# Kernel optimization log

Hardware: AMD Instinct MI355X
Metric: run time of the kernel (lower is better)

## Reference

```python
import jax, jax.numpy as jnp
import numpy as np

H, W = 256, 832            # full-res organized point cloud (HEIGHT/WIDTH globals)
STRIDE_H, STRIDE_W = 2, 4  # stride_H_list[0], stride_W_list[0]
OUT_H, OUT_W = 128, 208    # out_H_list[0], out_W_list[0]
KH, KW = 12, 20            # layer0 kernel_size
K = 32                     # layer0 K_sample


def _sa_layer(pts, h_idx, w_idx, w1, b1, w2, b2, w3, b3):
    """PointNet SA: strided center selection, window KNN grouping, MLP, max-pool.
    pts: (B,H,W,3); h_idx/w_idx: (M,) full-res grid coords of selected centers.
    """
    B = pts.shape[0]
    pts_flat = pts.reshape(B, H * W, 3)
    center_idx = h_idx * W + w_idx                      # (M,)
    centers = pts_flat[:, center_idx]                   # (B,M,3)  fast_select gather
    # candidate window around each center (clipped at borders)
    dh = jnp.arange(KH) - KH // 2
    dw = jnp.arange(KW) - KW // 2
    cand_h = jnp.clip(h_idx[:, None] + dh, 0, H - 1)    # (M,KH)
    cand_w = jnp.clip(w_idx[:, None] + dw, 0, W - 1)    # (M,KW)
    cand_idx = (cand_h[:, :, None] * W + cand_w[:, None, :]).reshape(-1, KH * KW)  # (M,P)
    cand = pts_flat[:, cand_idx]                        # (B,M,P,3) irregular gather
    d2 = jnp.sum((cand - centers[:, :, None, :]) ** 2, axis=-1)  # (B,M,P)
    _, nn = jax.lax.top_k(-d2, K)                       # K nearest within window
    knn = jnp.take_along_axis(cand, nn[..., None], axis=2)       # (B,M,K,3)
    rel = knn - centers[:, :, None, :]                  # local coordinates
    h = jax.nn.relu(rel @ w1 + b1)                      # mlp [8,8,16]
    h = jax.nn.relu(h @ w2 + b2)
    h = jax.nn.relu(h @ w3 + b3)
    return centers, jnp.max(h, axis=2)                  # (B,M,3), (B,M,16)


def setup_inputs() -> dict:
    key = jax.random.key(0)
    ks = jax.random.split(key, 5)
    return {
        "pos1": jax.random.normal(ks[0], (2, H, W, 3), jnp.float32) * 5.0,
        "pos2": jax.random.normal(ks[1], (2, H, W, 3), jnp.float32) * 5.0,
        "w1": jax.random.normal(ks[2], (3, 8), jnp.float32) * 0.3,
        "b1": jnp.zeros((8,), jnp.float32),
        "w2": jax.random.normal(ks[3], (8, 8), jnp.float32) * 0.3,
        "b2": jnp.zeros((8,), jnp.float32),
        "w3": jax.random.normal(ks[4], (8, 16), jnp.float32) * 0.3,
        "b3": jnp.zeros((16,), jnp.float32),
    }


def reference(pos1, pos2, w1, b1, w2, b2, w3, b3):
    # get_selected_idx for level 0: strided grid subsampling
    h_idx = jnp.repeat(jnp.arange(OUT_H) * STRIDE_H, OUT_W)  # (M,)
    w_idx = jnp.tile(jnp.arange(OUT_W) * STRIDE_W, OUT_H)    # (M,)
    _, f1 = _sa_layer(pos1, h_idx, w_idx, w1, b1, w2, b2, w3, b3)
    _, f2 = _sa_layer(pos2, h_idx, w_idx, w1, b1, w2, b2, w3, b3)
    return jnp.concatenate([f1, f2], axis=-1)  # (B, OUT_H*OUT_W, 32)
```

## Files before the change

kernel.cpp:

```cpp
#include <hip/hip_runtime.h>
#include <hip/hip_bf16.h>

#define HH 256
#define WW 832
#define OHH 128
#define OWW 208
#define NCAND 240
#define MM (OHH*OWW)

typedef float v2f __attribute__((ext_vector_type(2)));

__device__ __forceinline__ int iclamp(int v, int lo, int hi) { return min(max(v, lo), hi); }
__device__ __forceinline__ int mbcnt64(unsigned long long m) {
    return __builtin_amdgcn_mbcnt_hi((unsigned)(m >> 32),
           __builtin_amdgcn_mbcnt_lo((unsigned)(m & 0xFFFFFFFFull), 0));
}
__device__ __forceinline__ v2f sxor(v2f v, int m) {
    v2f r; r.x = __shfl_xor(v.x, m); r.y = __shfl_xor(v.y, m); return r;
}

__global__ void __launch_bounds__(256) sa_fused(
    const float* __restrict__ pos1, const float* __restrict__ pos2,
    const float* __restrict__ w1, const float* __restrict__ b1,
    const float* __restrict__ w2, const float* __restrict__ b2,
    const float* __restrict__ w3, const float* __restrict__ b3,
    float* __restrict__ out)
{
    __shared__ v2f sW1p[3][4];
    __shared__ v2f sW2p[8][4];
    __shared__ v2f sW3p[8][8];
    __shared__ v2f sB1p[4], sB2p[4], sB3p[8];
    __shared__ float4 selRel[128];
    __shared__ int tIdx[256];
    __shared__ int tHW[256];

    const int t = threadIdx.x;
    { int kh = (t * 205) >> 12; int kw = t - kh * 20;
      tHW[t]  = (kh << 16) | kw;
      tIdx[t] = (t < NCAND) ? (kh * WW + kw) * 3 : 0; }
    if (t < 12)              { int i = t >> 2,  op = t & 3;
        sW1p[i][op] = (v2f){w1[i*8 + 2*op], w1[i*8 + 2*op + 1]}; }
    if (t >= 16 && t < 48)   { int u = t - 16, i = u >> 2, op = u & 3;
        sW2p[i][op] = (v2f){w2[i*8 + 2*op], w2[i*8 + 2*op + 1]}; }
    if (t >= 64 && t < 128)  { int u = t - 64, i = u >> 3, op = u & 7;
        sW3p[i][op] = (v2f){w3[i*16 + 2*op], w3[i*16 + 2*op + 1]}; }
    if (t >= 128 && t < 132) { int u = t - 128; sB1p[u] = (v2f){b1[2*u], b1[2*u + 1]}; }
    if (t >= 132 && t < 136) { int u = t - 132; sB2p[u] = (v2f){b2[2*u], b2[2*u + 1]}; }
    if (t >= 136 && t < 144) { int u = t - 136; sB3p[u] = (v2f){b3[2*u], b3[2*u + 1]}; }
    __syncthreads();

    const int lane = t & 63;
    const int wid  = t >> 6;
    const int m    = blockIdx.x * 4 + wid;
    const int b    = blockIdx.y & 1;
    const int cl   = blockIdx.y >> 1;
    const float* __restrict__ base = (cl ? pos2 : pos1) + (size_t)b * (HH * WW * 3);

    const unsigned um = (unsigned)m;
    const int oh = (int)(um / OWW);
    const int ow = (int)(um - (unsigned)oh * OWW);
    const int h0 = oh * 2, w0 = ow * 4;

    const float cx = base[(h0 * WW + w0) * 3 + 0];
    const float cy = base[(h0 * WW + w0) * 3 + 1];
    const float cz = base[(h0 * WW + w0) * 3 + 2];

    unsigned d2b[4];
    float dxv[4], dyv[4], dzv[4];
    const bool interior = ((unsigned)(oh - 3) <= 122u) && ((unsigned)(ow - 3) <= 202u);
    if (interior) {
        const float* wbase = base + ((h0 - 6) * WW + (w0 - 10)) * 3;
        #pragma unroll
        for (int q = 0; q < 4; ++q) {
            const float* p = wbase + tIdx[q * 64 + lane];
            float dx = __fsub_rn(p[0], cx);
            float dy = __fsub_rn(p[1], cy);
            float dz = __fsub_rn(p[2], cz);
            dxv[q] = dx; dyv[q] = dy; dzv[q] = dz;
            d2b[q] = __float_as_uint(__fadd_rn(__fadd_rn(__fmul_rn(dx, dx), __fmul_rn(dy, dy)), __fmul_rn(dz, dz)));
        }
    } else {
        #pragma unroll
        for (int q = 0; q < 4; ++q) {
            int hw = tHW[q * 64 + lane];
            int ch = iclamp(h0 - 6 + (hw >> 16), 0, HH - 1);
            int cw = iclamp(w0 - 10 + (hw & 0xFFFF), 0, WW - 1);
            const float* p = base + (ch * WW + cw) * 3;
            float dx = __fsub_rn(p[0], cx);
            float dy = __fsub_rn(p[1], cy);
            float dz = __fsub_rn(p[2], cz);
            dxv[q] = dx; dyv[q] = dy; dzv[q] = dz;
            d2b[q] = __float_as_uint(__fadd_rn(__fadd_rn(__fmul_rn(dx, dx), __fmul_rn(dy, dy)), __fmul_rn(dz, dz)));
        }
    }
    if (lane >= 48) d2b[3] = 0xFFFFFFFFu;

    unsigned T = 0;
    unsigned long long sm0 = 0, sm1 = 0, sm2 = 0, sm3 = 0;
    bool exact = false;
    for (int bpos = 30; bpos >= 0; --bpos) {
        unsigned Q = T | (1u << bpos);
        unsigned long long t0 = __ballot(d2b[0] < Q);
        unsigned long long t1 = __ballot(d2b[1] < Q);
        unsigned long long t2 = __ballot(d2b[2] < Q);
        unsigned long long t3 = __ballot(d2b[3] < Q);
        int c = __popcll(t0) + __popcll(t1) + __popcll(t2) + __popcll(t3);
        if (c == 32) { sm0 = t0; sm1 = t1; sm2 = t2; sm3 = t3; exact = true; break; }
        if (c < 32) T = Q;
    }
    if (!exact) {
        unsigned long long l0 = __ballot(d2b[0] < T);
        unsigned long long l1 = __ballot(d2b[1] < T);
        unsigned long long l2 = __ballot(d2b[2] < T);
        unsigned long long l3 = __ballot(d2b[3] < T);
        unsigned long long e0 = __ballot(d2b[0] == T);
        unsigned long long e1 = __ballot(d2b[1] == T);
        unsigned long long e2 = __ballot(d2b[2] == T);
        unsigned long long e3 = __ballot(d2b[3] == T);
        int c_lt = __popcll(l0) + __popcll(l1) + __popcll(l2) + __popcll(l3);
        int r = 32 - c_lt;
        int p1 = __popcll(e0), p2 = p1 + __popcll(e1), p3 = p2 + __popcll(e2);
        bool s0 = (d2b[0] < T) || ((d2b[0] == T) && (mbcnt64(e0) < r));
        bool s1 = (d2b[1] < T) || ((d2b[1] == T) && (p1 + mbcnt64(e1) < r));
        bool s2 = (d2b[2] < T) || ((d2b[2] == T) && (p2 + mbcnt64(e2) < r));
        bool s3 = (d2b[3] < T) || ((d2b[3] == T) && (p3 + mbcnt64(e3) < r));
        sm0 = __ballot(s0); sm1 = __ballot(s1); sm2 = __ballot(s2); sm3 = __ballot(s3);
    }

    {
        int c1 = __popcll(sm0);
        int c2 = c1 + __popcll(sm1);
        int c3 = c2 + __popcll(sm2);
        int lb = wid * 32;
        if ((sm0 >> lane) & 1) selRel[lb +      mbcnt64(sm0)] = make_float4(dxv[0], dyv[0], dzv[0], 0.f);
        if ((sm1 >> lane) & 1) selRel[lb + c1 + mbcnt64(sm1)] = make_float4(dxv[1], dyv[1], dzv[1], 0.f);
        if ((sm2 >> lane) & 1) selRel[lb + c2 + mbcnt64(sm2)] = make_float4(dxv[2], dyv[2], dzv[2], 0.f);
        if ((sm3 >> lane) & 1) selRel[lb + c3 + mbcnt64(sm3)] = make_float4(dxv[3], dyv[3], dzv[3], 0.f);
    }
    asm volatile("s_waitcnt lgkmcnt(0)" ::: "memory");
    __builtin_amdgcn_sched_barrier(0);

    {
        float4 rel = selRel[wid * 32 + (lane & 31)];
        v2f rx2 = (v2f){rel.x, rel.x};
        v2f ry2 = (v2f){rel.y, rel.y};
        v2f rz2 = (v2f){rel.z, rel.z};

        v2f a1[4];
        #pragma unroll
        for (int op = 0; op < 4; ++op) {
            v2f a = sB1p[op];
            a = __builtin_elementwise_fma(rx2, sW1p[0][op], a);
            a = __builtin_elementwise_fma(ry2, sW1p[1][op], a);
            a = __builtin_elementwise_fma(rz2, sW1p[2][op], a);
            a1[op] = __builtin_elementwise_max(a, (v2f)(0.f));
        }
        v2f a2[4];
        #pragma unroll
        for (int op = 0; op < 4; ++op) a2[op] = sB2p[op];
        #pragma unroll
        for (int i = 0; i < 8; ++i) {
            float h = a1[i >> 1][i & 1];
            v2f hb = (v2f){h, h};
            #pragma unroll
            for (int op = 0; op < 4; ++op)
                a2[op] = __builtin_elementwise_fma(hb, sW2p[i][op], a2[op]);
        }
        #pragma unroll
        for (int op = 0; op < 4; ++op) a2[op] = __builtin_elementwise_max(a2[op], (v2f)(0.f));

        const int obp = (lane >> 5) << 2;
        v2f a3[4];
        #pragma unroll
        for (int op = 0; op < 4; ++op) a3[op] = sB3p[obp + op];
        #pragma unroll
        for (int i = 0; i < 8; ++i) {
            float h = a2[i >> 1][i & 1];
            v2f hb = (v2f){h, h};
            #pragma unroll
            for (int op = 0; op < 4; ++op)
                a3[op] = __builtin_elementwise_fma(hb, sW3p[i][obp + op], a3[op]);
        }

        #pragma unroll
        for (int step = 16; step >= 1; step >>= 1) {
            #pragma unroll
            for (int op = 0; op < 4; ++op)
                a3[op] = __builtin_elementwise_max(a3[op], sxor(a3[op], step));
        }
        if ((lane & 31) == 0) {
            #pragma unroll
            for (int op = 0; op < 4; ++op)
                a3[op] = __builtin_elementwise_max(a3[op], (v2f)(0.f));
            const int ob = (lane >> 5) << 3;
            float4* dst = (float4*)(out + ((size_t)(b * MM + m) * 32) + (size_t)cl * 16 + ob);
            dst[0] = make_float4(a3[0].x, a3[0].y, a3[1].x, a3[1].y);
            dst[1] = make_float4(a3[2].x, a3[2].y, a3[3].x, a3[3].y);
        }
    }
}

extern "C" void kernel_launch(void* const* d_in, const int* in_sizes, int n_in,
                              void* d_out, int out_size, void* d_ws, size_t ws_size,
                              hipStream_t stream) {
    const float* pos1 = (const float*)d_in[0];
    const float* pos2 = (const float*)d_in[1];
    const float* w1   = (const float*)d_in[2];
    const float* b1   = (const float*)d_in[3];
    const float* w2   = (const float*)d_in[4];
    const float* b2   = (const float*)d_in[5];
    const float* w3   = (const float*)d_in[6];
    const float* b3   = (const float*)d_in[7];
    float* out = (float*)d_out;

    dim3 grid(MM / 4, 4);
    sa_fused<<<grid, 256, 0, stream>>>(pos1, pos2, w1, b1, w2, b2, w3, b3, out);
}
```

Measured before the change: 100.8 us.

## Process two centers per wavefront with half-wave split radix select

Each 64-lane wavefront now handles two output centers, one per 32-lane half, with each lane holding 8 candidates instead of 4. The bitwise threshold search runs both halves together using split ballot popcounts, and each lane computes all 16 output channels for its center instead of splitting channels across halves. This halves the grid size and cuts the share of a wave spent on padded candidates and on the MLP duplicated across channel halves. In exchange it raises register pressure (8 candidates per lane, 16 accumulators) and the shared selection loop runs until the slower of the two centers finishes.

```diff
diff --git a/kernel.cpp b/kernel.cpp
--- a/kernel.cpp
+++ b/kernel.cpp
@@ -11,9 +11,8 @@
 typedef float v2f __attribute__((ext_vector_type(2)));
 
 __device__ __forceinline__ int iclamp(int v, int lo, int hi) { return min(max(v, lo), hi); }
-__device__ __forceinline__ int mbcnt64(unsigned long long m) {
-    return __builtin_amdgcn_mbcnt_hi((unsigned)(m >> 32),
-           __builtin_amdgcn_mbcnt_lo((unsigned)(m & 0xFFFFFFFFull), 0));
+__device__ __forceinline__ int mbcnt2(unsigned lo, unsigned hi) {
+    return __builtin_amdgcn_mbcnt_hi(hi, __builtin_amdgcn_mbcnt_lo(lo, 0));
 }
 __device__ __forceinline__ v2f sxor(v2f v, int m) {
     v2f r; r.x = __shfl_xor(v.x, m); r.y = __shfl_xor(v.y, m); return r;
@@ -30,14 +29,9 @@
     __shared__ v2f sW2p[8][4];
     __shared__ v2f sW3p[8][8];
     __shared__ v2f sB1p[4], sB2p[4], sB3p[8];
-    __shared__ float4 selRel[128];
-    __shared__ int tIdx[256];
-    __shared__ int tHW[256];
+    __shared__ float4 selRel[256];
 
     const int t = threadIdx.x;
-    { int kh = (t * 205) >> 12; int kw = t - kh * 20;
-      tHW[t]  = (kh << 16) | kw;
-      tIdx[t] = (t < NCAND) ? (kh * WW + kw) * 3 : 0; }
     if (t < 12)              { int i = t >> 2,  op = t & 3;
         sW1p[i][op] = (v2f){w1[i*8 + 2*op], w1[i*8 + 2*op + 1]}; }
     if (t >= 16 && t < 48)   { int u = t - 16, i = u >> 2, op = u & 3;
@@ -51,97 +45,118 @@
 
     const int lane = t & 63;
     const int wid  = t >> 6;
-    const int m    = blockIdx.x * 4 + wid;
+    const int l31  = lane & 31;
+    const int half = lane >> 5;
+    const int m    = blockIdx.x * 8 + wid * 2 + half;
     const int b    = blockIdx.y & 1;
     const int cl   = blockIdx.y >> 1;
     const float* __restrict__ base = (cl ? pos2 : pos1) + (size_t)b * (HH * WW * 3);
 
-    const unsigned um = (unsigned)m;
-    const int oh = (int)(um / OWW);
-    const int ow = (int)(um - (unsigned)oh * OWW);
+    const int oh = (int)(((unsigned)(m >> 4) * 5042u) >> 16);
+    const int ow = m - oh * OWW;
     const int h0 = oh * 2, w0 = ow * 4;
 
-    const float cx = base[(h0 * WW + w0) * 3 + 0];
-    const float cy = base[(h0 * WW + w0) * 3 + 1];
-    const float cz = base[(h0 * WW + w0) * 3 + 2];
-
-    unsigned d2b[4];
-    float dxv[4], dyv[4], dzv[4];
+    const int cidx = (h0 * WW + w0) * 3;
+    const float cx = base[cidx + 0];
+    const float cy = base[cidx + 1];
+    const float cz = base[cidx + 2];
+
+    unsigned d2b[8];
+    float rxv[8], ryv[8], rzv[8];
     const bool interior = ((unsigned)(oh - 3) <= 122u) && ((unsigned)(ow - 3) <= 202u);
-    if (interior) {
-        const float* wbase = base + ((h0 - 6) * WW + (w0 - 10)) * 3;
-        #pragma unroll
-        for (int q = 0; q < 4; ++q) {
-            const float* p = wbase + tIdx[q * 64 + lane];
+    const bool allInt = (__ballot(interior) == ~0ull);
+    if (allInt) {
+        const float* wb = base + ((h0 - 6) * WW + (w0 - 10)) * 3;
+        #pragma unroll
+        for (int r = 0; r < 8; ++r) {
+            int j = r * 32 + l31;
+            if (r == 7) j = min(j, NCAND - 1);
+            int kh = (j * 205) >> 12;
+            int kw = j - kh * 20;
+            const float* p = wb + (kh * WW + kw) * 3;
             float dx = __fsub_rn(p[0], cx);
             float dy = __fsub_rn(p[1], cy);
             float dz = __fsub_rn(p[2], cz);
-            dxv[q] = dx; dyv[q] = dy; dzv[q] = dz;
-            d2b[q] = __float_as_uint(__fadd_rn(__fadd_rn(__fmul_rn(dx, dx), __fmul_rn(dy, dy)), __fmul_rn(dz, dz)));
+            rxv[r] = dx; ryv[r] = dy; rzv[r] = dz;
+            d2b[r] = __float_as_uint(__fadd_rn(__fadd_rn(__fmul_rn(dx, dx), __fmul_rn(dy, dy)), __fmul_rn(dz, dz)));
         }
     } else {
         #pragma unroll
-        for (int q = 0; q < 4; ++q) {
-            int hw = tHW[q * 64 + lane];
-            int ch = iclamp(h0 - 6 + (hw >> 16), 0, HH - 1);
-            int cw = iclamp(w0 - 10 + (hw & 0xFFFF), 0, WW - 1);
+        for (int r = 0; r < 8; ++r) {
+            int j = r * 32 + l31;
+            if (r == 7) j = min(j, NCAND - 1);
+            int kh = (j * 205) >> 12;
+            int kw = j - kh * 20;
+            int ch = iclamp(h0 - 6 + kh, 0, HH - 1);
+            int cw = iclamp(w0 - 10 + kw, 0, WW - 1);
             const float* p = base + (ch * WW + cw) * 3;
             float dx = __fsub_rn(p[0], cx);
             float dy = __fsub_rn(p[1], cy);
             float dz = __fsub_rn(p[2], cz);
-            dxv[q] = dx; dyv[q] = dy; dzv[q] = dz;
-            d2b[q] = __float_as_uint(__fadd_rn(__fadd_rn(__fmul_rn(dx, dx), __fmul_rn(dy, dy)), __fmul_rn(dz, dz)));
-        }
-    }
-    if (lane >= 48) d2b[3] = 0xFFFFFFFFu;
-
-    unsigned T = 0;
-    unsigned long long sm0 = 0, sm1 = 0, sm2 = 0, sm3 = 0;
-    bool exact = false;
+            rxv[r] = dx; ryv[r] = dy; rzv[r] = dz;
+            d2b[r] = __float_as_uint(__fadd_rn(__fadd_rn(__fmul_rn(dx, dx), __fmul_rn(dy, dy)), __fmul_rn(dz, dz)));
+        }
+    }
+    if (l31 >= 16) d2b[7] = 0xFFFFFFFFu;
+
+    unsigned TA = 0, TB = 0;
+    bool doneA = false, doneB = false;
     for (int bpos = 30; bpos >= 0; --bpos) {
-        unsigned Q = T | (1u << bpos);
-        unsigned long long t0 = __ballot(d2b[0] < Q);
-        unsigned long long t1 = __ballot(d2b[1] < Q);
-        unsigned long long t2 = __ballot(d2b[2] < Q);
-        unsigned long long t3 = __ballot(d2b[3] < Q);
-        int c = __popcll(t0) + __popcll(t1) + __popcll(t2) + __popcll(t3);
-        if (c == 32) { sm0 = t0; sm1 = t1; sm2 = t2; sm3 = t3; exact = true; break; }
-        if (c < 32) T = Q;
-    }
-    if (!exact) {
-        unsigned long long l0 = __ballot(d2b[0] < T);
-        unsigned long long l1 = __ballot(d2b[1] < T);
-        unsigned long long l2 = __ballot(d2b[2] < T);
-        unsigned long long l3 = __ballot(d2b[3] < T);
-        unsigned long long e0 = __ballot(d2b[0] == T);
-        unsigned long long e1 = __ballot(d2b[1] == T);
-        unsigned long long e2 = __ballot(d2b[2] == T);
-        unsigned long long e3 = __ballot(d2b[3] == T);
-        int c_lt = __popcll(l0) + __popcll(l1) + __popcll(l2) + __popcll(l3);
-        int r = 32 - c_lt;
-        int p1 = __popcll(e0), p2 = p1 + __popcll(e1), p3 = p2 + __popcll(e2);
-        bool s0 = (d2b[0] < T) || ((d2b[0] == T) && (mbcnt64(e0) < r));
-        bool s1 = (d2b[1] < T) || ((d2b[1] == T) && (p1 + mbcnt64(e1) < r));
-        bool s2 = (d2b[2] < T) || ((d2b[2] == T) && (p2 + mbcnt64(e2) < r));
-        bool s3 = (d2b[3] < T) || ((d2b[3] == T) && (p3 + mbcnt64(e3) < r));
-        sm0 = __ballot(s0); sm1 = __ballot(s1); sm2 = __ballot(s2); sm3 = __ballot(s3);
-    }
+        unsigned QA = doneA ? TA : (TA | (1u << bpos));
+        unsigned QB = doneB ? TB : (TB | (1u << bpos));
+        unsigned Qv = half ? QB : QA;
+        unsigned long long m0 = __ballot(d2b[0] < Qv);
+        unsigned long long m1 = __ballot(d2b[1] < Qv);
+        unsigned long long m2 = __ballot(d2b[2] < Qv);
+        unsigned long long m3 = __ballot(d2b[3] < Qv);
+        unsigned long long m4 = __ballot(d2b[4] < Qv);
+        unsigned long long m5 = __ballot(d2b[5] < Qv);
+        unsigned long long m6 = __ballot(d2b[6] < Qv);
+        unsigned long long m7 = __ballot(d2b[7] < Qv);
+        int cA = __popc((unsigned)m0) + __popc((unsigned)m1) + __popc((unsigned)m2) + __popc((unsigned)m3)
+               + __popc((unsigned)m4) + __popc((unsigned)m5) + __popc((unsigned)m6) + __popc((unsigned)m7);
+        int cB = __popc((unsigned)(m0 >> 32)) + __popc((unsigned)(m1 >> 32)) + __popc((unsigned)(m2 >> 32)) + __popc((unsigned)(m3 >> 32))
+               + __popc((unsigned)(m4 >> 32)) + __popc((unsigned)(m5 >> 32)) + __popc((unsigned)(m6 >> 32)) + __popc((unsigned)(m7 >> 32));
+        if (!doneA) { if (cA == 32) { TA = QA; doneA = true; } else if (cA < 32) TA = QA; }
+        if (!doneB) { if (cB == 32) { TB = QB; doneB = true; } else if (cB < 32) TB = QB; }
+        if (doneA && doneB) break;
+    }
+
+    const unsigned Tv = half ? TB : TA;
+
+    int cltA = 0, cltB = 0;
+    #pragma unroll
+    for (int r = 0; r < 8; ++r) {
+        unsigned long long lm = __ballot(d2b[r] < Tv);
+        cltA += __popc((unsigned)lm);
+        cltB += __popc((unsigned)(lm >> 32));
+    }
+    const int rv = half ? (32 - cltB) : (32 - cltA);
+    const unsigned hmLo = half ? 0u : 0xFFFFFFFFu;
+    const unsigned hmHi = half ? 0xFFFFFFFFu : 0u;
 
     {
-        int c1 = __popcll(sm0);
-        int c2 = c1 + __popcll(sm1);
-        int c3 = c2 + __popcll(sm2);
-        int lb = wid * 32;
-        if ((sm0 >> lane) & 1) selRel[lb +      mbcnt64(sm0)] = make_float4(dxv[0], dyv[0], dzv[0], 0.f);
-        if ((sm1 >> lane) & 1) selRel[lb + c1 + mbcnt64(sm1)] = make_float4(dxv[1], dyv[1], dzv[1], 0.f);
-        if ((sm2 >> lane) & 1) selRel[lb + c2 + mbcnt64(sm2)] = make_float4(dxv[2], dyv[2], dzv[2], 0.f);
-        if ((sm3 >> lane) & 1) selRel[lb + c3 + mbcnt64(sm3)] = make_float4(dxv[3], dyv[3], dzv[3], 0.f);
+        int peA = 0, peB = 0, psA = 0, psB = 0;
+        #pragma unroll
+        for (int r = 0; r < 8; ++r) {
+            bool eqr = (d2b[r] == Tv);
+            unsigned long long em = __ballot(eqr);
+            int pe = half ? peB : peA;
+            bool tie = eqr && (pe + mbcnt2((unsigned)em & hmLo, (unsigned)(em >> 32) & hmHi) < rv);
+            bool mine = (d2b[r] < Tv) || tie;
+            unsigned long long sm = __ballot(mine);
+            int ps = half ? psB : psA;
+            int rank = ps + mbcnt2((unsigned)sm & hmLo, (unsigned)(sm >> 32) & hmHi);
+            if (mine) selRel[wid * 64 + half * 32 + rank] = make_float4(rxv[r], ryv[r], rzv[r], 0.f);
+            peA += __popc((unsigned)em);  peB += __popc((unsigned)(em >> 32));
+            psA += __popc((unsigned)sm);  psB += __popc((unsigned)(sm >> 32));
+        }
     }
     asm volatile("s_waitcnt lgkmcnt(0)" ::: "memory");
     __builtin_amdgcn_sched_barrier(0);
 
     {
-        float4 rel = selRel[wid * 32 + (lane & 31)];
+        float4 rel = selRel[wid * 64 + lane];
         v2f rx2 = (v2f){rel.x, rel.x};
         v2f ry2 = (v2f){rel.y, rel.y};
         v2f rz2 = (v2f){rel.z, rel.z};
@@ -169,33 +184,33 @@
         #pragma unroll
         for (int op = 0; op < 4; ++op) a2[op] = __builtin_elementwise_max(a2[op], (v2f)(0.f));
 
-        const int obp = (lane >> 5) << 2;
-        v2f a3[4];
-        #pragma unroll
-        for (int op = 0; op < 4; ++op) a3[op] = sB3p[obp + op];
+        v2f a3[8];
+        #pragma unroll
+        for (int op = 0; op < 8; ++op) a3[op] = sB3p[op];
         #pragma unroll
         for (int i = 0; i < 8; ++i) {
             float h = a2[i >> 1][i & 1];
             v2f hb = (v2f){h, h};
             #pragma unroll
-            for (int op = 0; op < 4; ++op)
-                a3[op] = __builtin_elementwise_fma(hb, sW3p[i][obp + op], a3[op]);
+            for (int op = 0; op < 8; ++op)
+                a3[op] = __builtin_elementwise_fma(hb, sW3p[i][op], a3[op]);
         }
 
         #pragma unroll
         for (int step = 16; step >= 1; step >>= 1) {
             #pragma unroll
-            for (int op = 0; op < 4; ++op)
+            for (int op = 0; op < 8; ++op)
                 a3[op] = __builtin_elementwise_max(a3[op], sxor(a3[op], step));
         }
-        if ((lane & 31) == 0) {
-            #pragma unroll
-            for (int op = 0; op < 4; ++op)
+        if (l31 == 0) {
+            #pragma unroll
+            for (int op = 0; op < 8; ++op)
                 a3[op] = __builtin_elementwise_max(a3[op], (v2f)(0.f));
-            const int ob = (lane >> 5) << 3;
-            float4* dst = (float4*)(out + ((size_t)(b * MM + m) * 32) + (size_t)cl * 16 + ob);
+            float4* dst = (float4*)(out + ((size_t)(b * MM + m) * 32) + (size_t)cl * 16);
             dst[0] = make_float4(a3[0].x, a3[0].y, a3[1].x, a3[1].y);
             dst[1] = make_float4(a3[2].x, a3[2].y, a3[3].x, a3[3].y);
+            dst[2] = make_float4(a3[4].x, a3[4].y, a3[5].x, a3[5].y);
+            dst[3] = make_float4(a3[6].x, a3[6].y, a3[7].x, a3[7].y);
         }
     }
 }
@@ -213,6 +228,6 @@
     const float* b3   = (const float*)d_in[7];
     float* out = (float*)d_out;
 
-    dim3 grid(MM / 4, 4);
+    dim3 grid(MM / 8, 4);
     sa_fused<<<grid, 256, 0, stream>>>(pos1, pos2, w1, b1, w2, b2, w3, b3, out);
 }
```

New measurement: 104.3 us. 1.03x slower.

## Remap window candidates per lane for vectorized loads and streamline top-K tie ballots

Applied to the files above, without the earlier changes.

Each lane now owns four consecutive points in one window row, so 60 lanes cover the 12x20 window. In the interior path the twelve contiguous floats are fetched with aligned float2/float4 loads instead of twelve scalar gathers. This also drops the shared-memory offset tables and their setup. The tie-resolution step now reuses the count from the radix search and ranks ties with per-lane mbcnt sums, which cuts the number of ballots. The risk is a different ordering among exactly tied candidates and more register pressure from the wider loads.

```diff
diff --git a/kernel.cpp b/kernel.cpp
--- a/kernel.cpp
+++ b/kernel.cpp
@@ -11,9 +11,9 @@
 typedef float v2f __attribute__((ext_vector_type(2)));
 
 __device__ __forceinline__ int iclamp(int v, int lo, int hi) { return min(max(v, lo), hi); }
-__device__ __forceinline__ int mbcnt64(unsigned long long m) {
+__device__ __forceinline__ int mbcnt2(unsigned long long m) {
     return __builtin_amdgcn_mbcnt_hi((unsigned)(m >> 32),
-           __builtin_amdgcn_mbcnt_lo((unsigned)(m & 0xFFFFFFFFull), 0));
+           __builtin_amdgcn_mbcnt_lo((unsigned)m, 0));
 }
 __device__ __forceinline__ v2f sxor(v2f v, int m) {
     v2f r; r.x = __shfl_xor(v.x, m); r.y = __shfl_xor(v.y, m); return r;
@@ -31,13 +31,8 @@
     __shared__ v2f sW3p[8][8];
     __shared__ v2f sB1p[4], sB2p[4], sB3p[8];
     __shared__ float4 selRel[128];
-    __shared__ int tIdx[256];
-    __shared__ int tHW[256];
 
     const int t = threadIdx.x;
-    { int kh = (t * 205) >> 12; int kw = t - kh * 20;
-      tHW[t]  = (kh << 16) | kw;
-      tIdx[t] = (t < NCAND) ? (kh * WW + kw) * 3 : 0; }
     if (t < 12)              { int i = t >> 2,  op = t & 3;
         sW1p[i][op] = (v2f){w1[i*8 + 2*op], w1[i*8 + 2*op + 1]}; }
     if (t >= 16 && t < 48)   { int u = t - 16, i = u >> 2, op = u & 3;
@@ -65,39 +60,46 @@
     const float cy = base[(h0 * WW + w0) * 3 + 1];
     const float cz = base[(h0 * WW + w0) * 3 + 2];
 
+    int kh  = (lane * 3277) >> 14;
+    int kwb = (lane - kh * 5) * 4;
+    if (lane >= 60) { kh = 11; kwb = 0; }
+
     unsigned d2b[4];
-    float dxv[4], dyv[4], dzv[4];
+    float rxv[4], ryv[4], rzv[4];
     const bool interior = ((unsigned)(oh - 3) <= 122u) && ((unsigned)(ow - 3) <= 202u);
     if (interior) {
-        const float* wbase = base + ((h0 - 6) * WW + (w0 - 10)) * 3;
+        const float* p = base + ((h0 - 6 + kh) * WW + (w0 - 10 + kwb)) * 3;
+        float2 Av = *(const float2*)(p);
+        float4 Bv = *(const float4*)(p + 2);
+        float4 Cv = *(const float4*)(p + 6);
+        float2 Dv = *(const float2*)(p + 10);
+        float px[4] = {Av.x, Bv.y, Cv.x, Cv.w};
+        float py[4] = {Av.y, Bv.z, Cv.y, Dv.x};
+        float pz[4] = {Bv.x, Bv.w, Cv.z, Dv.y};
         #pragma unroll
         for (int q = 0; q < 4; ++q) {
-            const float* p = wbase + tIdx[q * 64 + lane];
+            float dx = __fsub_rn(px[q], cx);
+            float dy = __fsub_rn(py[q], cy);
+            float dz = __fsub_rn(pz[q], cz);
+            rxv[q] = dx; ryv[q] = dy; rzv[q] = dz;
+            d2b[q] = __float_as_uint(__fadd_rn(__fadd_rn(__fmul_rn(dx, dx), __fmul_rn(dy, dy)), __fmul_rn(dz, dz)));
+        }
+    } else {
+        int chh = iclamp(h0 - 6 + kh, 0, HH - 1);
+        #pragma unroll
+        for (int q = 0; q < 4; ++q) {
+            int cw = iclamp(w0 - 10 + kwb + q, 0, WW - 1);
+            const float* p = base + (chh * WW + cw) * 3;
             float dx = __fsub_rn(p[0], cx);
             float dy = __fsub_rn(p[1], cy);
             float dz = __fsub_rn(p[2], cz);
-            dxv[q] = dx; dyv[q] = dy; dzv[q] = dz;
+            rxv[q] = dx; ryv[q] = dy; rzv[q] = dz;
             d2b[q] = __float_as_uint(__fadd_rn(__fadd_rn(__fmul_rn(dx, dx), __fmul_rn(dy, dy)), __fmul_rn(dz, dz)));
         }
-    } else {
-        #pragma unroll
-        for (int q = 0; q < 4; ++q) {
-            int hw = tHW[q * 64 + lane];
-            int ch = iclamp(h0 - 6 + (hw >> 16), 0, HH - 1);
-            int cw = iclamp(w0 - 10 + (hw & 0xFFFF), 0, WW - 1);
-            const float* p = base + (ch * WW + cw) * 3;
-            float dx = __fsub_rn(p[0], cx);
-            float dy = __fsub_rn(p[1], cy);
-            float dz = __fsub_rn(p[2], cz);
-            dxv[q] = dx; dyv[q] = dy; dzv[q] = dz;
-            d2b[q] = __float_as_uint(__fadd_rn(__fadd_rn(__fmul_rn(dx, dx), __fmul_rn(dy, dy)), __fmul_rn(dz, dz)));
-        }
-    }
-    if (lane >= 48) d2b[3] = 0xFFFFFFFFu;
-
-    unsigned T = 0;
-    unsigned long long sm0 = 0, sm1 = 0, sm2 = 0, sm3 = 0;
-    bool exact = false;
+    }
+    if (lane >= 60) { d2b[0] = d2b[1] = d2b[2] = d2b[3] = 0xFFFFFFFFu; }
+
+    unsigned T = 0; int c0 = 0; bool exact = false;
     for (int bpos = 30; bpos >= 0; --bpos) {
         unsigned Q = T | (1u << bpos);
         unsigned long long t0 = __ballot(d2b[0] < Q);
@@ -105,37 +107,43 @@
         unsigned long long t2 = __ballot(d2b[2] < Q);
         unsigned long long t3 = __ballot(d2b[3] < Q);
         int c = __popcll(t0) + __popcll(t1) + __popcll(t2) + __popcll(t3);
-        if (c == 32) { sm0 = t0; sm1 = t1; sm2 = t2; sm3 = t3; exact = true; break; }
-        if (c < 32) T = Q;
-    }
+        if (c == 32) { T = Q; c0 = 32; exact = true; break; }
+        if (c < 32)  { T = Q; c0 = c; }
+    }
+
+    bool tie0 = false, tie1 = false, tie2 = false, tie3 = false;
     if (!exact) {
-        unsigned long long l0 = __ballot(d2b[0] < T);
-        unsigned long long l1 = __ballot(d2b[1] < T);
-        unsigned long long l2 = __ballot(d2b[2] < T);
-        unsigned long long l3 = __ballot(d2b[3] < T);
-        unsigned long long e0 = __ballot(d2b[0] == T);
-        unsigned long long e1 = __ballot(d2b[1] == T);
-        unsigned long long e2 = __ballot(d2b[2] == T);
-        unsigned long long e3 = __ballot(d2b[3] == T);
-        int c_lt = __popcll(l0) + __popcll(l1) + __popcll(l2) + __popcll(l3);
-        int r = 32 - c_lt;
-        int p1 = __popcll(e0), p2 = p1 + __popcll(e1), p3 = p2 + __popcll(e2);
-        bool s0 = (d2b[0] < T) || ((d2b[0] == T) && (mbcnt64(e0) < r));
-        bool s1 = (d2b[1] < T) || ((d2b[1] == T) && (p1 + mbcnt64(e1) < r));
-        bool s2 = (d2b[2] < T) || ((d2b[2] == T) && (p2 + mbcnt64(e2) < r));
-        bool s3 = (d2b[3] < T) || ((d2b[3] == T) && (p3 + mbcnt64(e3) < r));
-        sm0 = __ballot(s0); sm1 = __ballot(s1); sm2 = __ballot(s2); sm3 = __ballot(s3);
+        const int r = 32 - c0;
+        bool eq0 = (d2b[0] == T), eq1 = (d2b[1] == T), eq2 = (d2b[2] == T), eq3 = (d2b[3] == T);
+        unsigned long long e0 = __ballot(eq0);
+        unsigned long long e1 = __ballot(eq1);
+        unsigned long long e2 = __ballot(eq2);
+        unsigned long long e3 = __ballot(eq3);
+        int SA = mbcnt2(e0) + mbcnt2(e1) + mbcnt2(e2) + mbcnt2(e3);
+        int E1 = (int)eq0, E2 = E1 + (int)eq1, E3 = E2 + (int)eq2;
+        tie0 = eq0 && (SA      < r);
+        tie1 = eq1 && (SA + E1 < r);
+        tie2 = eq2 && (SA + E2 < r);
+        tie3 = eq3 && (SA + E3 < r);
     }
 
     {
-        int c1 = __popcll(sm0);
-        int c2 = c1 + __popcll(sm1);
-        int c3 = c2 + __popcll(sm2);
+        bool m0 = (d2b[0] < T) || tie0;
+        bool m1 = (d2b[1] < T) || tie1;
+        bool m2 = (d2b[2] < T) || tie2;
+        bool m3 = (d2b[3] < T) || tie3;
+        unsigned long long s0 = __ballot(m0);
+        unsigned long long s1 = __ballot(m1);
+        unsigned long long s2 = __ballot(m2);
+        unsigned long long s3 = __ballot(m3);
+        int p1 = __popcll(s0);
+        int p2 = p1 + __popcll(s1);
+        int p3 = p2 + __popcll(s2);
         int lb = wid * 32;
-        if ((sm0 >> lane) & 1) selRel[lb +      mbcnt64(sm0)] = make_float4(dxv[0], dyv[0], dzv[0], 0.f);
-        if ((sm1 >> lane) & 1) selRel[lb + c1 + mbcnt64(sm1)] = make_float4(dxv[1], dyv[1], dzv[1], 0.f);
-        if ((sm2 >> lane) & 1) selRel[lb + c2 + mbcnt64(sm2)] = make_float4(dxv[2], dyv[2], dzv[2], 0.f);
-        if ((sm3 >> lane) & 1) selRel[lb + c3 + mbcnt64(sm3)] = make_float4(dxv[3], dyv[3], dzv[3], 0.f);
+        if (m0) selRel[lb +      mbcnt2(s0)] = make_float4(rxv[0], ryv[0], rzv[0], 0.f);
+        if (m1) selRel[lb + p1 + mbcnt2(s1)] = make_float4(rxv[1], ryv[1], rzv[1], 0.f);
+        if (m2) selRel[lb + p2 + mbcnt2(s2)] = make_float4(rxv[2], ryv[2], rzv[2], 0.f);
+        if (m3) selRel[lb + p3 + mbcnt2(s3)] = make_float4(rxv[3], ryv[3], rzv[3], 0.f);
     }
     asm volatile("s_waitcnt lgkmcnt(0)" ::: "memory");
     __builtin_amdgcn_sched_barrier(0);
```

New measurement: 94.95 us. -5.8%, faster.
